# Kernel tuning notes

Hardware: AMD Instinct MI355X
Metric: run time of the kernel (lower is better)

Reference implementation:

```python
import jax, jax.numpy as jnp
import numpy as np

S, D, H, E, A = 30, 200, 200, 1024, 6
B, T = 1024, 64


def setup_inputs() -> dict:
    key = jax.random.key(0)
    ks = jax.random.split(key, 32)
    rn = lambda k, sh, sc=0.05: jax.random.normal(k, sh, dtype=jnp.float32) * sc
    inp = {
        'embed': rn(ks[0], (B, T, E), 1.0),
        'action': rn(ks[1], (B, T, A), 1.0),
        'noise_prior': rn(ks[2], (T, B, S), 1.0),
        'noise_post': rn(ks[3], (T, B, S), 1.0),
        # img1: Dense(hidden) on [stoch+action]
        'w_img1': rn(ks[4], (S + A, H)), 'b_img1': jnp.zeros((H,), jnp.float32),
        # GRUCell(deter): kernel [in,3*D] (z,r,h order), recurrent kernel, 2 biases (reset_after=True)
        'gru_w': rn(ks[5], (H, 3 * D)), 'gru_u': rn(ks[6], (D, 3 * D)),
        'gru_b': jnp.zeros((3 * D,), jnp.float32), 'gru_rb': jnp.zeros((3 * D,), jnp.float32),
        'w_img2': rn(ks[7], (D, H)), 'b_img2': jnp.zeros((H,), jnp.float32),
        'w_imean': rn(ks[8], (H, S)), 'b_imean': jnp.zeros((S,), jnp.float32),
        'w_istd': rn(ks[9], (H, S)), 'b_istd': jnp.zeros((S,), jnp.float32),
        # obs1: Dense(hidden) on [deter+embed]
        'w_obs1': rn(ks[10], (D + E, H)), 'b_obs1': jnp.zeros((H,), jnp.float32),
        'w_omean': rn(ks[11], (H, S)), 'b_omean': jnp.zeros((S,), jnp.float32),
        'w_ostd': rn(ks[12], (H, S)), 'b_ostd': jnp.zeros((S,), jnp.float32),
    }
    return inp


def _observe(embed, action, noise_prior, noise_post,
             w_img1, b_img1, gru_w, gru_u, gru_b, gru_rb,
             w_img2, b_img2, w_imean, b_imean, w_istd, b_istd,
             w_obs1, b_obs1, w_omean, b_omean, w_ostd, b_ostd):
    elu = jax.nn.elu
    Bsz = action.shape[0]

    def step(carry, xs):
        stoch, deter = carry  # [B,S], [B,D]
        a, e, nz_p, nz_o = xs
        # ---- img_step (prior) ----
        x = elu(jnp.concatenate([stoch, a], -1) @ w_img1 + b_img1)  # [B,H]
        xg = x @ gru_w + gru_b          # [B,3D]
        hg = deter @ gru_u + gru_rb     # [B,3D] (reset_after)
        xz, xr, xh = jnp.split(xg, 3, -1)
        hz, hr, hh = jnp.split(hg, 3, -1)
        z = jax.nn.sigmoid(xz + hz)
        r = jax.nn.sigmoid(xr + hr)
        hhat = jnp.tanh(xh + r * hh)
        deter_n = z * deter + (1.0 - z) * hhat  # [B,D]
        x2 = elu(deter_n @ w_img2 + b_img2)
        pmean = x2 @ w_imean + b_imean
        pstd = jax.nn.softplus(x2 @ w_istd + b_istd) + 0.1
        pstoch = pmean + pstd * nz_p
        # ---- obs_step (posterior) ----
        xo = elu(jnp.concatenate([deter_n, e], -1) @ w_obs1 + b_obs1)
        omean = xo @ w_omean + b_omean
        ostd = jax.nn.softplus(xo @ w_ostd + b_ostd)
        ostoch = omean + ostd * nz_o
        out = jnp.concatenate([omean, ostd, ostoch, deter_n,
                               pmean, pstd, pstoch, deter_n], -1)  # [B, 580]
        return (ostoch, deter_n), out

    init = (jnp.zeros((Bsz, S), embed.dtype), jnp.zeros((Bsz, D), embed.dtype))
    xs = (jnp.transpose(action, (1, 0, 2)), jnp.transpose(embed, (1, 0, 2)),
          noise_prior, noise_post)
    _, ys = jax.lax.scan(step, init, xs)  # [T,B,580]
    return jnp.transpose(ys, (1, 0, 2))   # [B,T,580] = post(mean,std,stoch,deter) ++ prior(...)


def reference(embed, action, noise_prior, noise_post,
              w_img1, b_img1, gru_w, gru_u, gru_b, gru_rb,
              w_img2, b_img2, w_imean, b_imean, w_istd, b_istd,
              w_obs1, b_obs1, w_omean, b_omean, w_ostd, b_ostd):
    return _observe(embed, action, noise_prior, noise_post,
                    w_img1, b_img1, gru_w, gru_u, gru_b, gru_rb,
                    w_img2, b_img2, w_imean, b_imean, w_istd, b_istd,
                    w_obs1, b_obs1, w_omean, b_omean, w_ostd, b_ostd)
```

## Files before the change

### kernel.cpp

```cpp
#include <hip/hip_runtime.h>
#include <cstddef>


typedef __bf16 bf16x8 __attribute__((ext_vector_type(8)));
typedef float  f32x4  __attribute__((ext_vector_type(4)));

#define OFF_K1WT 0
#define OFF_W1F  212992
#define OFF_GWF  226304
#define OFF_GUF  362496
#define OFF_WCF  498688
#define OFF_WHF  591872
#define WS_BF_TOTAL 620544
#define WS_XPRE_BYTES 1241088

__device__ __forceinline__ float elu1(float v){ return v > 0.f ? v : expm1f(v); }
__device__ __forceinline__ float sigm(float v){ return 1.f / (1.f + expf(-v)); }
__device__ __forceinline__ float spls(float v){ return fmaxf(v,0.f) + log1pf(expf(-fabsf(v))); }

__global__ __launch_bounds__(256) void k0_convert(
    const float* __restrict__ w_img1, const float* __restrict__ gru_w,
    const float* __restrict__ gru_u,  const float* __restrict__ w_img2,
    const float* __restrict__ w_imean, const float* __restrict__ w_istd,
    const float* __restrict__ w_obs1, const float* __restrict__ w_omean,
    const float* __restrict__ w_ostd, __bf16* __restrict__ o)
{
  int i = blockIdx.x * 256 + threadIdx.x;
  if (i >= WS_BF_TOTAL) return;
  float v = 0.f;
  if (i < OFF_W1F) {
    int n = i >> 10, k = i & 1023;
    v = (n < 200) ? w_obs1[(size_t)(200 + k) * 200 + n] : 0.f;
  } else if (i < OFF_GWF) {
    int q = i - OFF_W1F;
    int e = q & 7, lane = (q >> 3) & 63, f = q >> 9;
    int kc = f & 1, tt = f >> 1;
    int n  = tt * 16 + (lane & 15);
    int kk = kc * 32 + (lane >> 4) * 8 + e;
    if (n < 200 && kk < 36) v = w_img1[kk * 200 + n];
  } else if (i < OFF_GUF) {
    int q = i - OFF_GWF;
    int e = q & 7, lane = (q >> 3) & 63, f = q >> 9;
    int k = f % 7, tt = f / 7;
    int j  = tt * 16 + (lane & 15);
    int kk = k * 32 + (lane >> 4) * 8 + e;
    if (j < 600 && kk < 200) v = gru_w[kk * 600 + j];
  } else if (i < OFF_WCF) {
    int q = i - OFF_GUF;
    int e = q & 7, lane = (q >> 3) & 63, f = q >> 9;
    int k = f % 7, tt = f / 7;
    int j  = tt * 16 + (lane & 15);
    int kk = k * 32 + (lane >> 4) * 8 + e;
    if (j < 600 && kk < 200) v = gru_u[kk * 600 + j];
  } else if (i < OFF_WHF) {
    int q = i - OFF_WCF;
    int e = q & 7, lane = (q >> 3) & 63, f = q >> 9;
    int k = f % 7, tt = f / 7;
    int kk = k * 32 + (lane >> 4) * 8 + e;
    if (kk < 200) {
      if (tt < 13) {
        int n = tt * 16 + (lane & 15);
        if (n < 200) v = w_img2[kk * 200 + n];
      } else {
        int n = (tt - 13) * 16 + (lane & 15);
        if (n < 200) v = w_obs1[kk * 200 + n];
      }
    }
  } else {
    int q = i - OFF_WHF;
    int e = q & 7, lane = (q >> 3) & 63, f = q >> 9;
    int k = f % 7, tt = f / 7;
    int kk = k * 32 + (lane >> 4) * 8 + e;
    int n = tt * 16 + (lane & 15);
    int h = n >> 5, c = n & 31;
    if (kk < 200 && c < 30) {
      const float* wh = (h == 0) ? w_omean : (h == 1) ? w_ostd : (h == 2) ? w_imean : w_istd;
      v = wh[kk * 30 + c];
    }
  }
  o[i] = (__bf16)v;
}

__global__ __launch_bounds__(256) void k1_embed_gemm(
    const float* __restrict__ embed, const __bf16* __restrict__ wT,
    const float* __restrict__ b_obs1, float* __restrict__ xpre)
{
  __shared__ __align__(16) __bf16 As[64][72];
  __shared__ __align__(16) __bf16 Bs[208][72];
  int tid = threadIdx.x;
  int b = blockIdx.x;
  int wave = tid >> 6, lane = tid & 63;
  int lm = lane & 15, quad = lane >> 4;

  f32x4 acc[13];
#pragma unroll
  for (int n = 0; n < 13; ++n) acc[n] = (f32x4){0.f, 0.f, 0.f, 0.f};

  const float* arow_base = embed + (size_t)b * 64 * 1024;

  for (int ko = 0; ko < 1024; ko += 64) {
#pragma unroll
    for (int p = 0; p < 4; ++p) {
      int v = p * 256 + tid; int row = v >> 4; int c4 = v & 15;
      float4 f = *(const float4*)(arow_base + (size_t)row * 1024 + ko + c4 * 4);
      __bf16* dst = &As[row][c4 * 4];
      dst[0] = (__bf16)f.x; dst[1] = (__bf16)f.y;
      dst[2] = (__bf16)f.z; dst[3] = (__bf16)f.w;
    }
#pragma unroll
    for (int p = 0; p < 13; ++p) {
      int v = p * 256 + tid; int n = v >> 4; int c4 = v & 15;
      ushort4 u = *(const ushort4*)(wT + (size_t)n * 1024 + ko + c4 * 4);
      *(ushort4*)&Bs[n][c4 * 4] = u;
    }
    __syncthreads();
#pragma unroll
    for (int kc = 0; kc < 2; ++kc) {
      bf16x8 a = *(const bf16x8*)&As[16 * wave + lm][kc * 32 + quad * 8];
#pragma unroll
      for (int n = 0; n < 13; ++n) {
        bf16x8 bb = *(const bf16x8*)&Bs[16 * n + lm][kc * 32 + quad * 8];
        acc[n] = __builtin_amdgcn_mfma_f32_16x16x32_bf16(a, bb, acc[n], 0, 0, 0);
      }
    }
    __syncthreads();
  }
  int trow_base = 16 * wave + quad * 4;
#pragma unroll
  for (int n = 0; n < 13; ++n) {
    int col = n * 16 + lm;
    if (col < 200) {
      float bias = b_obs1[col];
#pragma unroll
      for (int r = 0; r < 4; ++r) {
        int trow = trow_base + r;
        xpre[(size_t)trow * (1024 * 200) + (size_t)b * 200 + col] = acc[n][r] + bias;
      }
    }
  }
}

__global__ __launch_bounds__(1024) void k2_recurrent(
    const float* __restrict__ action, const float* __restrict__ noise_prior,
    const float* __restrict__ noise_post,
    const float* __restrict__ b_img1, const float* __restrict__ gru_b,
    const float* __restrict__ gru_rb, const float* __restrict__ b_img2,
    const float* __restrict__ b_imean, const float* __restrict__ b_istd,
    const float* __restrict__ b_omean, const float* __restrict__ b_ostd,
    const __bf16* __restrict__ w1F, const __bf16* __restrict__ gwF,
    const __bf16* __restrict__ guF, const __bf16* __restrict__ wcF,
    const __bf16* __restrict__ whF,
    const float* __restrict__ xpre, float* __restrict__ out)
{
  __shared__ __align__(16) __bf16 actin[16][72];
  __shared__ __align__(16) __bf16 xbuf[16][232];
  __shared__ __align__(16) __bf16 dbuf[16][232];
  __shared__ __align__(16) char   ovl[39168];
  __shared__ float biasL[1760];
  __shared__ float noiseb[960];

  const int tid  = threadIdx.x;
  const int wv   = tid >> 6;
  const int lane = tid & 63;
  const int lm   = lane & 15, quad = lane >> 4;
  const int b0   = blockIdx.x * 16;

  __bf16* gg    = (__bf16*)ovl;
  __bf16* x2b   = (__bf16*)ovl;
  __bf16* xob   = (__bf16*)(ovl + 7424);
  float*  headb = (float*)(ovl + 14848);

  for (int i = tid; i < 16 * 72; i += 1024) {
    int m = i / 72, c = i - m * 72;
    if (c < 30 || c >= 36) actin[m][c] = (__bf16)0.f;
  }
  for (int i = tid; i < 16 * 232; i += 1024) { ((__bf16*)xbuf)[i] = (__bf16)0.f; ((__bf16*)dbuf)[i] = (__bf16)0.f; }
  for (int i = tid; i < 1760; i += 1024) {
    float v = 0.f;
    if (i < 208)       { if (i < 200) v = b_img1[i]; }
    else if (i < 816)  { int j = i - 208;  if (j < 600) v = gru_b[j]; }
    else if (i < 1424) { int j = i - 816;  if (j < 600) v = gru_rb[j]; }
    else if (i < 1632) { int j = i - 1424; if (j < 200) v = b_img2[j]; }
    else { int n = i - 1632; int h = n >> 5, c = n & 31;
           if (c < 30) v = ((h == 0) ? b_omean : (h == 1) ? b_ostd : (h == 2) ? b_imean : b_istd)[c]; }
    biasL[i] = v;
  }
  if (tid < 96) {
    int m = tid / 6, k = tid - m * 6;
    actin[m][30 + k] = (__bf16)action[(size_t)(b0 + m) * 384 + k];
  }
  __syncthreads();

  for (int t = 0; t < 64; ++t) {
    if (wv < 13) {
      const __bf16* bw = w1F + wv * 1024 + lane * 8;
      bf16x8 a0 = *(const bf16x8*)&actin[lm][quad * 8];
      bf16x8 a1 = *(const bf16x8*)&actin[lm][32 + quad * 8];
      bf16x8 bv0 = *(const bf16x8*)(bw);
      bf16x8 bv1 = *(const bf16x8*)(bw + 512);
      f32x4 c = (f32x4){0.f, 0.f, 0.f, 0.f};
      c = __builtin_amdgcn_mfma_f32_16x16x32_bf16(a0, bv0, c, 0, 0, 0);
      c = __builtin_amdgcn_mfma_f32_16x16x32_bf16(a1, bv1, c, 0, 0, 0);
      int col = wv * 16 + lm;
      float bias = biasL[col];
      if (col < 200) {
#pragma unroll
        for (int r = 0; r < 4; ++r) xbuf[quad * 4 + r][col] = (__bf16)elu1(c[r] + bias);
      }
    } else {
      int j = (wv - 13) * 64 + lane;
      const float* np = noise_post  + (size_t)t * 30720 + (size_t)b0 * 30;
      const float* nq = noise_prior + (size_t)t * 30720 + (size_t)b0 * 30;
      for (int q = j; q < 480; q += 192) {
        noiseb[q]       = np[q];
        noiseb[480 + q] = nq[q];
      }
    }
    __syncthreads();

    float xp[4] = {0.f, 0.f, 0.f, 0.f};
    {
      int tt_xo = (wv >= 13) ? wv : (wv < 10 ? wv + 16 : -1);
      if (tt_xo >= 0) {
        int col0 = (tt_xo - 13) * 16 + lm;
        if (col0 < 200) {
#pragma unroll
          for (int r = 0; r < 4; ++r)
            xp[r] = xpre[((size_t)t * 1024 + b0 + quad * 4 + r) * 200 + col0];
        }
      }
    }

    {
      const int gsel = wv >> 3, wsub = wv & 7;
      const __bf16* WF    = gsel ? guF : gwF;
      const __bf16* Abase = gsel ? &dbuf[0][0] : &xbuf[0][0];
      const int cbase = gsel ? 608 : 0;
      const int bbase = gsel ? 816 : 208;
      bf16x8 af[7];
#pragma unroll
      for (int k = 0; k < 7; ++k) af[k] = *(const bf16x8*)(Abase + lm * 232 + k * 32 + quad * 8);
      bf16x8 cur[7], nxt[7];
      {
        const __bf16* bw = WF + (size_t)wsub * 3584 + lane * 8;
#pragma unroll
        for (int k = 0; k < 7; ++k) cur[k] = *(const bf16x8*)(bw + k * 512);
      }
      for (int tt = wsub; tt < 38; tt += 8) {
        int tn = tt + 8;
        if (tn < 38) {
          const __bf16* bn = WF + (size_t)tn * 3584 + lane * 8;
#pragma unroll
          for (int k = 0; k < 7; ++k) nxt[k] = *(const bf16x8*)(bn + k * 512);
        }
        f32x4 c0 = (f32x4){0.f, 0.f, 0.f, 0.f};
        f32x4 c1 = (f32x4){0.f, 0.f, 0.f, 0.f};
        c0 = __builtin_amdgcn_mfma_f32_16x16x32_bf16(af[0], cur[0], c0, 0, 0, 0);
        c1 = __builtin_amdgcn_mfma_f32_16x16x32_bf16(af[1], cur[1], c1, 0, 0, 0);
        c0 = __builtin_amdgcn_mfma_f32_16x16x32_bf16(af[2], cur[2], c0, 0, 0, 0);
        c1 = __builtin_amdgcn_mfma_f32_16x16x32_bf16(af[3], cur[3], c1, 0, 0, 0);
        c0 = __builtin_amdgcn_mfma_f32_16x16x32_bf16(af[4], cur[4], c0, 0, 0, 0);
        c1 = __builtin_amdgcn_mfma_f32_16x16x32_bf16(af[5], cur[5], c1, 0, 0, 0);
        c0 = __builtin_amdgcn_mfma_f32_16x16x32_bf16(af[6], cur[6], c0, 0, 0, 0);
        f32x4 c = c0 + c1;
        int col = tt * 16 + lm;
        float bias = biasL[bbase + col];
#pragma unroll
        for (int r = 0; r < 4; ++r) gg[(quad * 4 + r) * 1224 + cbase + col] = (__bf16)(c[r] + bias);
#pragma unroll
        for (int k = 0; k < 7; ++k) cur[k] = nxt[k];
      }
    }
    __syncthreads();

    for (int idx = tid; idx < 3200; idx += 1024) {
      int m = idx / 200, d = idx - m * 200;
      const __bf16* row = gg + m * 1224;
      float xz = (float)row[d],        xr_ = (float)row[200 + d], xh = (float)row[400 + d];
      float hz = (float)row[608 + d],  hr_ = (float)row[808 + d], hh = (float)row[1008 + d];
      float z  = sigm(xz + hz);
      float rr = sigm(xr_ + hr_);
      float hc = 2.f * sigm(2.f * (xh + rr * hh)) - 1.f;
      float dn = z * (float)dbuf[m][d] + (1.f - z) * hc;
      dbuf[m][d] = (__bf16)dn;
      size_t ob = ((size_t)(b0 + m) * 64 + t) * 580;
      out[ob + 90 + d]  = dn;
      out[ob + 380 + d] = dn;
    }
    __syncthreads();

    {
      bf16x8 df[7];
#pragma unroll
      for (int k = 0; k < 7; ++k) df[k] = *(const bf16x8*)(&dbuf[lm][0] + k * 32 + quad * 8);
      for (int tt = wv; tt < 26; tt += 16) {
        const __bf16* bw = wcF + (size_t)tt * 3584 + lane * 8;
        bf16x8 bv[7];
#pragma unroll
        for (int k = 0; k < 7; ++k) bv[k] = *(const bf16x8*)(bw + k * 512);
        f32x4 c0 = (f32x4){0.f, 0.f, 0.f, 0.f};
        f32x4 c1 = (f32x4){0.f, 0.f, 0.f, 0.f};
        c0 = __builtin_amdgcn_mfma_f32_16x16x32_bf16(df[0], bv[0], c0, 0, 0, 0);
        c1 = __builtin_amdgcn_mfma_f32_16x16x32_bf16(df[1], bv[1], c1, 0, 0, 0);
        c0 = __builtin_amdgcn_mfma_f32_16x16x32_bf16(df[2], bv[2], c0, 0, 0, 0);
        c1 = __builtin_amdgcn_mfma_f32_16x16x32_bf16(df[3], bv[3], c1, 0, 0, 0);
        c0 = __builtin_amdgcn_mfma_f32_16x16x32_bf16(df[4], bv[4], c0, 0, 0, 0);
        c1 = __builtin_amdgcn_mfma_f32_16x16x32_bf16(df[5], bv[5], c1, 0, 0, 0);
        c0 = __builtin_amdgcn_mfma_f32_16x16x32_bf16(df[6], bv[6], c0, 0, 0, 0);
        f32x4 c = c0 + c1;
        if (tt < 13) {
          int col = tt * 16 + lm;
          float bias = biasL[1424 + col];
          if (col < 200) {
#pragma unroll
            for (int r = 0; r < 4; ++r) x2b[(quad * 4 + r) * 232 + col] = (__bf16)elu1(c[r] + bias);
          }
        } else {
          int col = (tt - 13) * 16 + lm;
          if (col < 200) {
#pragma unroll
            for (int r = 0; r < 4; ++r) {
              int m2 = quad * 4 + r;
              xob[m2 * 232 + col] = (__bf16)elu1(c[r] + xp[r]);
            }
          }
        }
      }
    }
    __syncthreads();

    if (wv < 8) {
      const __bf16* Ab = (wv < 4) ? xob : x2b;
      bf16x8 hf[7];
#pragma unroll
      for (int k = 0; k < 7; ++k) hf[k] = *(const bf16x8*)(Ab + lm * 232 + k * 32 + quad * 8);
      const __bf16* bw = whF + wv * 3584 + lane * 8;
      bf16x8 bv[7];
#pragma unroll
      for (int k = 0; k < 7; ++k) bv[k] = *(const bf16x8*)(bw + k * 512);
      f32x4 c0 = (f32x4){0.f, 0.f, 0.f, 0.f};
      f32x4 c1 = (f32x4){0.f, 0.f, 0.f, 0.f};
      c0 = __builtin_amdgcn_mfma_f32_16x16x32_bf16(hf[0], bv[0], c0, 0, 0, 0);
      c1 = __builtin_amdgcn_mfma_f32_16x16x32_bf16(hf[1], bv[1], c1, 0, 0, 0);
      c0 = __builtin_amdgcn_mfma_f32_16x16x32_bf16(hf[2], bv[2], c0, 0, 0, 0);
      c1 = __builtin_amdgcn_mfma_f32_16x16x32_bf16(hf[3], bv[3], c1, 0, 0, 0);
      c0 = __builtin_amdgcn_mfma_f32_16x16x32_bf16(hf[4], bv[4], c0, 0, 0, 0);
      c1 = __builtin_amdgcn_mfma_f32_16x16x32_bf16(hf[5], bv[5], c1, 0, 0, 0);
      c0 = __builtin_amdgcn_mfma_f32_16x16x32_bf16(hf[6], bv[6], c0, 0, 0, 0);
      f32x4 c = c0 + c1;
      int n = wv * 16 + lm;
      float bias = biasL[1632 + n];
#pragma unroll
      for (int r = 0; r < 4; ++r) headb[(quad * 4 + r) * 132 + n] = c[r] + bias;
    }
    __syncthreads();

    if (tid < 480) {
      int m = tid / 30, c = tid - m * 30;
      const float* hb = headb + m * 132;
      float om = hb[c], osr = hb[32 + c], pm = hb[64 + c], psr = hb[96 + c];
      float os = spls(osr);
      float ps = spls(psr) + 0.1f;
      float nzo = noiseb[tid];
      float nzp = noiseb[480 + tid];
      float ost = om + os * nzo;
      float pst = pm + ps * nzp;
      actin[m][c] = (__bf16)ost;
      size_t ob = ((size_t)(b0 + m) * 64 + t) * 580;
      out[ob + c]       = om;
      out[ob + 30 + c]  = os;
      out[ob + 60 + c]  = ost;
      out[ob + 290 + c] = pm;
      out[ob + 320 + c] = ps;
      out[ob + 350 + c] = pst;
    } else if (tid < 576 && t < 63) {
      int j = tid - 480;
      int m = j / 6, k = j - m * 6;
      actin[m][30 + k] = (__bf16)action[(size_t)(b0 + m) * 384 + (t + 1) * 6 + k];
    }
    __syncthreads();
  }
}

extern "C" void kernel_launch(void* const* d_in, const int* in_sizes, int n_in,
                              void* d_out, int out_size, void* d_ws, size_t ws_size,
                              hipStream_t stream) {
  const float* embed   = (const float*)d_in[0];
  const float* action  = (const float*)d_in[1];
  const float* nzp     = (const float*)d_in[2];
  const float* nzo     = (const float*)d_in[3];
  const float* w_img1  = (const float*)d_in[4];
  const float* b_img1  = (const float*)d_in[5];
  const float* gru_w   = (const float*)d_in[6];
  const float* gru_u   = (const float*)d_in[7];
  const float* gru_b   = (const float*)d_in[8];
  const float* gru_rb  = (const float*)d_in[9];
  const float* w_img2  = (const float*)d_in[10];
  const float* b_img2  = (const float*)d_in[11];
  const float* w_imean = (const float*)d_in[12];
  const float* b_imean = (const float*)d_in[13];
  const float* w_istd  = (const float*)d_in[14];
  const float* b_istd  = (const float*)d_in[15];
  const float* w_obs1  = (const float*)d_in[16];
  const float* b_obs1  = (const float*)d_in[17];
  const float* w_omean = (const float*)d_in[18];
  const float* b_omean = (const float*)d_in[19];
  const float* w_ostd  = (const float*)d_in[20];
  const float* b_ostd  = (const float*)d_in[21];
  float* out = (float*)d_out;

  __bf16* wbf = (__bf16*)d_ws;
  float* xpre = (float*)((char*)d_ws + WS_XPRE_BYTES);

  k0_convert<<<(WS_BF_TOTAL + 255) / 256, 256, 0, stream>>>(
      w_img1, gru_w, gru_u, w_img2, w_imean, w_istd, w_obs1, w_omean, w_ostd, wbf);

  k1_embed_gemm<<<1024, 256, 0, stream>>>(embed, wbf + OFF_K1WT, b_obs1, xpre);

  k2_recurrent<<<64, 1024, 0, stream>>>(
      action, nzp, nzo,
      b_img1, gru_b, gru_rb, b_img2, b_imean, b_istd, b_omean, b_ostd,
      wbf + OFF_W1F, wbf + OFF_GWF, wbf + OFF_GUF, wbf + OFF_WCF, wbf + OFF_WHF,
      xpre, out);
}
```

Measured before the change: 1.517 ms.

## Split recurrent kernel to 4 batch rows per block across 256 blocks

Each recurrent block now handles 4 batch rows instead of 16 and the grid grows from 64 to 256 blocks, so all CUs take part in the serial time loop. The small img1 and head weights are staged once in shared memory. The GRU and obs1 weight fragment loads are issued before the barriers so they overlap with earlier phases. The cost is that each 16-row MFMA tile is only a quarter used, so more weight traffic is paid per useful row, and shared memory per block grows.

```diff
diff --git a/kernel.cpp b/kernel.cpp
--- a/kernel.cpp
+++ b/kernel.cpp
@@ -156,14 +156,16 @@
   __shared__ __align__(16) __bf16 xbuf[16][232];
   __shared__ __align__(16) __bf16 dbuf[16][232];
   __shared__ __align__(16) char   ovl[39168];
+  __shared__ __align__(16) __bf16 w1L[13312];
+  __shared__ __align__(16) __bf16 whL[28672];
   __shared__ float biasL[1760];
-  __shared__ float noiseb[960];
+  __shared__ float noiseb[240];
 
   const int tid  = threadIdx.x;
   const int wv   = tid >> 6;
   const int lane = tid & 63;
   const int lm   = lane & 15, quad = lane >> 4;
-  const int b0   = blockIdx.x * 16;
+  const int b0   = blockIdx.x * 4;
 
   __bf16* gg    = (__bf16*)ovl;
   __bf16* x2b   = (__bf16*)ovl;
@@ -175,6 +177,8 @@
     if (c < 30 || c >= 36) actin[m][c] = (__bf16)0.f;
   }
   for (int i = tid; i < 16 * 232; i += 1024) { ((__bf16*)xbuf)[i] = (__bf16)0.f; ((__bf16*)dbuf)[i] = (__bf16)0.f; }
+  for (int i = tid; i < 1664; i += 1024) ((uint4*)w1L)[i] = ((const uint4*)w1F)[i];
+  for (int i = tid; i < 3584; i += 1024) ((uint4*)whL)[i] = ((const uint4*)whF)[i];
   for (int i = tid; i < 1760; i += 1024) {
     float v = 0.f;
     if (i < 208)       { if (i < 200) v = b_img1[i]; }
@@ -185,15 +189,24 @@
            if (c < 30) v = ((h == 0) ? b_omean : (h == 1) ? b_ostd : (h == 2) ? b_imean : b_istd)[c]; }
     biasL[i] = v;
   }
-  if (tid < 96) {
+  if (tid < 24) {
     int m = tid / 6, k = tid - m * 6;
     actin[m][30 + k] = (__bf16)action[(size_t)(b0 + m) * 384 + k];
   }
   __syncthreads();
 
   for (int t = 0; t < 64; ++t) {
+    const int gsel = wv >> 3, wsub = wv & 7;
+    const __bf16* WF = gsel ? guF : gwF;
+    bf16x8 cur[7];
+    {
+      const __bf16* bw = WF + (size_t)wsub * 3584 + lane * 8;
+#pragma unroll
+      for (int k = 0; k < 7; ++k) cur[k] = *(const bf16x8*)(bw + k * 512);
+    }
+
     if (wv < 13) {
-      const __bf16* bw = w1F + wv * 1024 + lane * 8;
+      const __bf16* bw = &w1L[wv * 1024 + lane * 8];
       bf16x8 a0 = *(const bf16x8*)&actin[lm][quad * 8];
       bf16x8 a1 = *(const bf16x8*)&actin[lm][32 + quad * 8];
       bf16x8 bv0 = *(const bf16x8*)(bw);
@@ -203,17 +216,16 @@
       c = __builtin_amdgcn_mfma_f32_16x16x32_bf16(a1, bv1, c, 0, 0, 0);
       int col = wv * 16 + lm;
       float bias = biasL[col];
-      if (col < 200) {
-#pragma unroll
-        for (int r = 0; r < 4; ++r) xbuf[quad * 4 + r][col] = (__bf16)elu1(c[r] + bias);
-      }
-    } else {
-      int j = (wv - 13) * 64 + lane;
+      if (col < 200 && quad == 0) {
+#pragma unroll
+        for (int r = 0; r < 4; ++r) xbuf[r][col] = (__bf16)elu1(c[r] + bias);
+      }
+    } else if (wv == 13) {
       const float* np = noise_post  + (size_t)t * 30720 + (size_t)b0 * 30;
       const float* nq = noise_prior + (size_t)t * 30720 + (size_t)b0 * 30;
-      for (int q = j; q < 480; q += 192) {
+      for (int q = lane; q < 120; q += 64) {
         noiseb[q]       = np[q];
-        noiseb[480 + q] = nq[q];
+        noiseb[120 + q] = nq[q];
       }
     }
     __syncthreads();
@@ -221,31 +233,24 @@
     float xp[4] = {0.f, 0.f, 0.f, 0.f};
     {
       int tt_xo = (wv >= 13) ? wv : (wv < 10 ? wv + 16 : -1);
-      if (tt_xo >= 0) {
+      if (tt_xo >= 0 && quad == 0) {
         int col0 = (tt_xo - 13) * 16 + lm;
         if (col0 < 200) {
 #pragma unroll
           for (int r = 0; r < 4; ++r)
-            xp[r] = xpre[((size_t)t * 1024 + b0 + quad * 4 + r) * 200 + col0];
+            xp[r] = xpre[((size_t)t * 1024 + b0 + r) * 200 + col0];
         }
       }
     }
 
     {
-      const int gsel = wv >> 3, wsub = wv & 7;
-      const __bf16* WF    = gsel ? guF : gwF;
       const __bf16* Abase = gsel ? &dbuf[0][0] : &xbuf[0][0];
       const int cbase = gsel ? 608 : 0;
       const int bbase = gsel ? 816 : 208;
       bf16x8 af[7];
 #pragma unroll
       for (int k = 0; k < 7; ++k) af[k] = *(const bf16x8*)(Abase + lm * 232 + k * 32 + quad * 8);
-      bf16x8 cur[7], nxt[7];
-      {
-        const __bf16* bw = WF + (size_t)wsub * 3584 + lane * 8;
-#pragma unroll
-        for (int k = 0; k < 7; ++k) cur[k] = *(const bf16x8*)(bw + k * 512);
-      }
+      bf16x8 nxt[7];
       for (int tt = wsub; tt < 38; tt += 8) {
         int tn = tt + 8;
         if (tn < 38) {
@@ -263,18 +268,27 @@
         c1 = __builtin_amdgcn_mfma_f32_16x16x32_bf16(af[5], cur[5], c1, 0, 0, 0);
         c0 = __builtin_amdgcn_mfma_f32_16x16x32_bf16(af[6], cur[6], c0, 0, 0, 0);
         f32x4 c = c0 + c1;
-        int col = tt * 16 + lm;
-        float bias = biasL[bbase + col];
-#pragma unroll
-        for (int r = 0; r < 4; ++r) gg[(quad * 4 + r) * 1224 + cbase + col] = (__bf16)(c[r] + bias);
+        if (quad == 0) {
+          int col = tt * 16 + lm;
+          float bias = biasL[bbase + col];
+#pragma unroll
+          for (int r = 0; r < 4; ++r) gg[r * 1224 + cbase + col] = (__bf16)(c[r] + bias);
+        }
 #pragma unroll
         for (int k = 0; k < 7; ++k) cur[k] = nxt[k];
       }
     }
     __syncthreads();
 
-    for (int idx = tid; idx < 3200; idx += 1024) {
-      int m = idx / 200, d = idx - m * 200;
+    bf16x8 pf[7];
+    {
+      const __bf16* bw = wcF + (size_t)wv * 3584 + lane * 8;
+#pragma unroll
+      for (int k = 0; k < 7; ++k) pf[k] = *(const bf16x8*)(bw + k * 512);
+    }
+
+    if (tid < 800) {
+      int m = tid / 200, d = tid - m * 200;
       const __bf16* row = gg + m * 1224;
       float xz = (float)row[d],        xr_ = (float)row[200 + d], xh = (float)row[400 + d];
       float hz = (float)row[608 + d],  hr_ = (float)row[808 + d], hh = (float)row[1008 + d];
@@ -293,7 +307,38 @@
       bf16x8 df[7];
 #pragma unroll
       for (int k = 0; k < 7; ++k) df[k] = *(const bf16x8*)(&dbuf[lm][0] + k * 32 + quad * 8);
-      for (int tt = wv; tt < 26; tt += 16) {
+
+      {
+        int tt = wv;
+        f32x4 c0 = (f32x4){0.f, 0.f, 0.f, 0.f};
+        f32x4 c1 = (f32x4){0.f, 0.f, 0.f, 0.f};
+        c0 = __builtin_amdgcn_mfma_f32_16x16x32_bf16(df[0], pf[0], c0, 0, 0, 0);
+        c1 = __builtin_amdgcn_mfma_f32_16x16x32_bf16(df[1], pf[1], c1, 0, 0, 0);
+        c0 = __builtin_amdgcn_mfma_f32_16x16x32_bf16(df[2], pf[2], c0, 0, 0, 0);
+        c1 = __builtin_amdgcn_mfma_f32_16x16x32_bf16(df[3], pf[3], c1, 0, 0, 0);
+        c0 = __builtin_amdgcn_mfma_f32_16x16x32_bf16(df[4], pf[4], c0, 0, 0, 0);
+        c1 = __builtin_amdgcn_mfma_f32_16x16x32_bf16(df[5], pf[5], c1, 0, 0, 0);
+        c0 = __builtin_amdgcn_mfma_f32_16x16x32_bf16(df[6], pf[6], c0, 0, 0, 0);
+        f32x4 c = c0 + c1;
+        if (quad == 0) {
+          if (tt < 13) {
+            int col = tt * 16 + lm;
+            float bias = biasL[1424 + col];
+            if (col < 200) {
+#pragma unroll
+              for (int r = 0; r < 4; ++r) x2b[r * 232 + col] = (__bf16)elu1(c[r] + bias);
+            }
+          } else {
+            int col = (tt - 13) * 16 + lm;
+            if (col < 200) {
+#pragma unroll
+              for (int r = 0; r < 4; ++r) xob[r * 232 + col] = (__bf16)elu1(c[r] + xp[r]);
+            }
+          }
+        }
+      }
+      if (wv < 10) {
+        int tt = wv + 16;
         const __bf16* bw = wcF + (size_t)tt * 3584 + lane * 8;
         bf16x8 bv[7];
 #pragma unroll
@@ -308,21 +353,11 @@
         c1 = __builtin_amdgcn_mfma_f32_16x16x32_bf16(df[5], bv[5], c1, 0, 0, 0);
         c0 = __builtin_amdgcn_mfma_f32_16x16x32_bf16(df[6], bv[6], c0, 0, 0, 0);
         f32x4 c = c0 + c1;
-        if (tt < 13) {
-          int col = tt * 16 + lm;
-          float bias = biasL[1424 + col];
-          if (col < 200) {
-#pragma unroll
-            for (int r = 0; r < 4; ++r) x2b[(quad * 4 + r) * 232 + col] = (__bf16)elu1(c[r] + bias);
-          }
-        } else {
+        if (quad == 0) {
           int col = (tt - 13) * 16 + lm;
           if (col < 200) {
 #pragma unroll
-            for (int r = 0; r < 4; ++r) {
-              int m2 = quad * 4 + r;
-              xob[m2 * 232 + col] = (__bf16)elu1(c[r] + xp[r]);
-            }
+            for (int r = 0; r < 4; ++r) xob[r * 232 + col] = (__bf16)elu1(c[r] + xp[r]);
           }
         }
       }
@@ -334,7 +369,7 @@
       bf16x8 hf[7];
 #pragma unroll
       for (int k = 0; k < 7; ++k) hf[k] = *(const bf16x8*)(Ab + lm * 232 + k * 32 + quad * 8);
-      const __bf16* bw = whF + wv * 3584 + lane * 8;
+      const __bf16* bw = &whL[wv * 3584 + lane * 8];
       bf16x8 bv[7];
 #pragma unroll
       for (int k = 0; k < 7; ++k) bv[k] = *(const bf16x8*)(bw + k * 512);
@@ -348,21 +383,23 @@
       c1 = __builtin_amdgcn_mfma_f32_16x16x32_bf16(hf[5], bv[5], c1, 0, 0, 0);
       c0 = __builtin_amdgcn_mfma_f32_16x16x32_bf16(hf[6], bv[6], c0, 0, 0, 0);
       f32x4 c = c0 + c1;
-      int n = wv * 16 + lm;
-      float bias = biasL[1632 + n];
-#pragma unroll
-      for (int r = 0; r < 4; ++r) headb[(quad * 4 + r) * 132 + n] = c[r] + bias;
-    }
-    __syncthreads();
-
-    if (tid < 480) {
+      if (quad == 0) {
+        int n = wv * 16 + lm;
+        float bias = biasL[1632 + n];
+#pragma unroll
+        for (int r = 0; r < 4; ++r) headb[r * 132 + n] = c[r] + bias;
+      }
+    }
+    __syncthreads();
+
+    if (tid < 120) {
       int m = tid / 30, c = tid - m * 30;
       const float* hb = headb + m * 132;
       float om = hb[c], osr = hb[32 + c], pm = hb[64 + c], psr = hb[96 + c];
       float os = spls(osr);
       float ps = spls(psr) + 0.1f;
       float nzo = noiseb[tid];
-      float nzp = noiseb[480 + tid];
+      float nzp = noiseb[120 + tid];
       float ost = om + os * nzo;
       float pst = pm + ps * nzp;
       actin[m][c] = (__bf16)ost;
@@ -373,8 +410,8 @@
       out[ob + 290 + c] = pm;
       out[ob + 320 + c] = ps;
       out[ob + 350 + c] = pst;
-    } else if (tid < 576 && t < 63) {
-      int j = tid - 480;
+    } else if (tid >= 120 && tid < 144 && t < 63) {
+      int j = tid - 120;
       int m = j / 6, k = j - m * 6;
       actin[m][30 + k] = (__bf16)action[(size_t)(b0 + m) * 384 + (t + 1) * 6 + k];
     }
@@ -417,7 +454,7 @@
 
   k1_embed_gemm<<<1024, 256, 0, stream>>>(embed, wbf + OFF_K1WT, b_obs1, xpre);
 
-  k2_recurrent<<<64, 1024, 0, stream>>>(
+  k2_recurrent<<<256, 1024, 0, stream>>>(
       action, nzp, nzo,
       b_img1, gru_b, gru_rb, b_img2, b_imean, b_istd, b_omean, b_ostd,
       wbf + OFF_W1F, wbf + OFF_GWF, wbf + OFF_GUF, wbf + OFF_WCF, wbf + OFF_WHF,
```

After: 1.682 ms. 10.9% more time.
